# Kernel optimization log

Hardware: AMD Instinct MI355X
Metric: run time of the kernel (lower is better)

## Reference

```python
import jax, jax.numpy as jnp
import numpy as np

COMMITMENT_COST = 0.25


def setup_inputs() -> dict:
    key = jax.random.key(0)
    k1, k2 = jax.random.split(key)
    z = jax.random.normal(k1, (64, 256, 32, 32), dtype=jnp.float32)
    codebook = jax.random.normal(k2, (512, 256), dtype=jnp.float32) * 0.02
    return {"z": z, "codebook": codebook}


def reference(z, codebook):
    B, C, H, W = z.shape
    # [B,C,H,W] -> [B*H*W, C]
    z_flat = jnp.transpose(z, (0, 2, 3, 1)).reshape(-1, C)
    # squared euclidean distances via matmul expansion (same argmin as broadcast form)
    d = (
        jnp.sum(z_flat * z_flat, axis=-1, keepdims=True)
        - 2.0 * (z_flat @ codebook.T)
        + jnp.sum(codebook * codebook, axis=-1)
    )  # [N, num_codes]
    encoding_indices = jnp.argmin(d, axis=1)  # [N]
    z_q = codebook[encoding_indices].reshape(B, H, W, C)
    z_q = jnp.transpose(z_q, (0, 3, 1, 2))  # [B,C,H,W]
    commitment_loss = COMMITMENT_COST * jnp.mean(
        (jax.lax.stop_gradient(z_q) - z) ** 2
    )
    embedding_loss = jnp.mean((z_q - jax.lax.stop_gradient(z)) ** 2)
    loss = commitment_loss + embedding_loss
    # straight-through estimator
    z_q_st = z + jax.lax.stop_gradient(z_q - z)
    return z_q_st, encoding_indices, loss
```

## Files before the change

### kernel.cpp

```cpp
#include <hip/hip_runtime.h>

#define C_DIM   256
#define K_CODES 512
#define N_POS   65536
#define OUT0_ELEMS 16777216
#define OUT1_ELEMS 65536

__global__ __launch_bounds__(256) void vq_transpose_kernel(const float* __restrict__ cb,
                                                           float* __restrict__ cbT)
{
    const int k = blockIdx.x;
    const int c = threadIdx.x;
    cbT[c * K_CODES + k] = cb[k * C_DIM + c];
}

__global__ __launch_bounds__(256) void vq_cc_kernel(const float* __restrict__ cbT,
                                                    float* __restrict__ cc)
{
    const int k = blockIdx.x * 256 + threadIdx.x;
    float s1[8], s2[8];
    #pragma unroll
    for (int j = 0; j < 8; ++j) { s1[j] = 0.f; s2[j] = 0.f; }
    for (int c8 = 0; c8 < 16; ++c8) {
        #pragma unroll
        for (int j = 0; j < 8; ++j) {
            float v = cbT[(c8 * 8 + j) * K_CODES + k];
            s1[j] = __fadd_rn(s1[j], __fmul_rn(v, v));
        }
    }
    for (int c8 = 16; c8 < 32; ++c8) {
        #pragma unroll
        for (int j = 0; j < 8; ++j) {
            float v = cbT[(c8 * 8 + j) * K_CODES + k];
            s2[j] = __fadd_rn(s2[j], __fmul_rn(v, v));
        }
    }
    float b1 = __fadd_rn(__fadd_rn(__fadd_rn(s1[0], s1[1]), __fadd_rn(s1[2], s1[3])),
                         __fadd_rn(__fadd_rn(s1[4], s1[5]), __fadd_rn(s1[6], s1[7])));
    float b2 = __fadd_rn(__fadd_rn(__fadd_rn(s2[0], s2[1]), __fadd_rn(s2[2], s2[3])),
                         __fadd_rn(__fadd_rn(s2[4], s2[5]), __fadd_rn(s2[6], s2[7])));
    cc[k] = __fadd_rn(b1, b2);
}

__global__ __launch_bounds__(256) void vq_zz_kernel(const float* __restrict__ z,
                                                    float* __restrict__ zz)
{
    const int pos = blockIdx.x * 256 + threadIdx.x;
    const float* zp = z + ((size_t)(pos >> 10) << 18) + (pos & 1023);
    float s1[8], s2[8];
    #pragma unroll
    for (int j = 0; j < 8; ++j) { s1[j] = 0.f; s2[j] = 0.f; }
    for (int c8 = 0; c8 < 16; ++c8) {
        #pragma unroll
        for (int j = 0; j < 8; ++j) {
            float v = zp[(size_t)(c8 * 8 + j) << 10];
            s1[j] = __fadd_rn(s1[j], __fmul_rn(v, v));
        }
    }
    for (int c8 = 16; c8 < 32; ++c8) {
        #pragma unroll
        for (int j = 0; j < 8; ++j) {
            float v = zp[(size_t)(c8 * 8 + j) << 10];
            s2[j] = __fadd_rn(s2[j], __fmul_rn(v, v));
        }
    }
    float b1 = __fadd_rn(__fadd_rn(__fadd_rn(s1[0], s1[1]), __fadd_rn(s1[2], s1[3])),
                         __fadd_rn(__fadd_rn(s1[4], s1[5]), __fadd_rn(s1[6], s1[7])));
    float b2 = __fadd_rn(__fadd_rn(__fadd_rn(s2[0], s2[1]), __fadd_rn(s2[2], s2[3])),
                         __fadd_rn(__fadd_rn(s2[4], s2[5]), __fadd_rn(s2[6], s2[7])));
    zz[pos] = __fadd_rn(b1, b2);
}

__global__ __launch_bounds__(256) void vq_main_kernel(
    const float* __restrict__ z, const float* __restrict__ cbT,
    const float* __restrict__ ccv, const float* __restrict__ zzbuf,
    float* __restrict__ bd, int* __restrict__ bc)
{
    const int blk   = blockIdx.x;
    const int cg    = blk & 3;
    const int chunk = blk >> 2;
    const int b     = chunk >> 3;
    const int hw0   = (chunk & 7) << 7;
    const int tid   = threadIdx.x;
    const int lane  = tid & 63;
    const int w     = tid >> 6;

    const float* zp = z + ((size_t)b << 18) + hw0 + lane;
    const int cb0   = __builtin_amdgcn_readfirstlane((cg << 7) + (w << 5));
    const float* cbbase = cbT + cb0;

    float acc[2][32];
    #pragma unroll
    for (int p = 0; p < 2; ++p)
        #pragma unroll
        for (int k = 0; k < 32; ++k) acc[p][k] = 0.f;

    for (int c = 0; c < C_DIM; ++c) {
        const float* zc = zp + ((size_t)c << 10);
        const float zv0 = zc[0];
        const float zv1 = zc[64];
        const float* cbrow = cbbase + (c << 9);
        #pragma unroll
        for (int k = 0; k < 32; ++k) {
            const float cv = cbrow[k];
            acc[0][k] = __builtin_fmaf(zv0, cv, acc[0][k]);
            acc[1][k] = __builtin_fmaf(zv1, cv, acc[1][k]);
        }
    }

    __shared__ float sdm[4][2][64];
    __shared__ int   sco[4][2][64];

    const float* ccp = ccv + cb0;
    const int posb = (b << 10) + hw0 + lane;
    #pragma unroll
    for (int p = 0; p < 2; ++p) {
        const float zzv = zzbuf[posb + p * 64];
        float bestd = 3.4e38f;
        int   bestc = cb0;
        #pragma unroll
        for (int k = 0; k < 32; ++k) {
            float d = __fadd_rn(__fsub_rn(zzv, __fmul_rn(2.0f, acc[p][k])), ccp[k]);
            if (d < bestd) { bestd = d; bestc = cb0 + k; }
        }
        sdm[w][p][lane] = bestd;
        sco[w][p][lane] = bestc;
    }
    __syncthreads();

    if (w == 0) {
        #pragma unroll
        for (int p = 0; p < 2; ++p) {
            float bdv = sdm[0][p][lane];
            int   bcv = sco[0][p][lane];
            #pragma unroll
            for (int ww = 1; ww < 4; ++ww) {
                float d2 = sdm[ww][p][lane];
                int   c2 = sco[ww][p][lane];
                if (d2 < bdv || (d2 == bdv && c2 < bcv)) { bdv = d2; bcv = c2; }
            }
            bd[(cg << 16) + posb + p * 64] = bdv;
            bc[(cg << 16) + posb + p * 64] = bcv;
        }
    }
}

__global__ __launch_bounds__(256) void vq_combine_kernel(
    const float* __restrict__ bd, const int* __restrict__ bc,
    int* __restrict__ idx, float* __restrict__ out1, float* __restrict__ partials)
{
    const int t   = threadIdx.x;
    const int pos = blockIdx.x * 256 + t;
    float bdv = bd[pos];
    int   bcv = bc[pos];
    #pragma unroll
    for (int g = 1; g < 4; ++g) {
        float d2 = bd[(g << 16) + pos];
        int   c2 = bc[(g << 16) + pos];
        if (d2 < bdv || (d2 == bdv && c2 < bcv)) { bdv = d2; bcv = c2; }
    }
    idx[pos]  = bcv;
    out1[pos] = (float)bcv;

    __shared__ float s[256];
    s[t] = bdv;
    __syncthreads();
    for (int off = 128; off > 0; off >>= 1) {
        if (t < off) s[t] += s[t + off];
        __syncthreads();
    }
    if (t == 0) partials[blockIdx.x] = s[0];
}

__global__ __launch_bounds__(256) void vq_gather_kernel(
    const float* __restrict__ cb, const int* __restrict__ idx,
    float* __restrict__ out0)
{
    const int blk = blockIdx.x;
    const int b   = blk >> 4;
    const int hw0 = (blk & 15) << 6;
    const int lane = threadIdx.x & 63;
    const int w    = threadIdx.x >> 6;

    __shared__ int sidx[64];
    if (threadIdx.x < 64) sidx[threadIdx.x] = idx[(blk << 6) + threadIdx.x];
    __syncthreads();

    const int code = sidx[lane];
    const float4* crow4 = reinterpret_cast<const float4*>(cb + ((size_t)code << 8) + (w << 6));
    float* ob = out0 + ((size_t)b << 18) + ((size_t)(w * 64) << 10) + hw0 + lane;
    #pragma unroll 4
    for (int j4 = 0; j4 < 16; ++j4) {
        float4 v = crow4[j4];
        ob[(size_t)(j4 * 4 + 0) << 10] = v.x;
        ob[(size_t)(j4 * 4 + 1) << 10] = v.y;
        ob[(size_t)(j4 * 4 + 2) << 10] = v.z;
        ob[(size_t)(j4 * 4 + 3) << 10] = v.w;
    }
}

__global__ __launch_bounds__(256) void vq_finalize_kernel(
    const float* __restrict__ partials, float* __restrict__ out2)
{
    __shared__ float s[256];
    const int t = threadIdx.x;
    s[t] = partials[t];
    __syncthreads();
    for (int off = 128; off > 0; off >>= 1) {
        if (t < off) s[t] += s[t + off];
        __syncthreads();
    }
    if (t == 0)
        out2[0] = 1.25f * (s[0] * (1.0f / 16777216.0f));
}

extern "C" void kernel_launch(void* const* d_in, const int* in_sizes, int n_in,
                              void* d_out, int out_size, void* d_ws, size_t ws_size,
                              hipStream_t stream)
{
    const float* z  = (const float*)d_in[0];
    const float* cb = (const float*)d_in[1];

    float* out0 = (float*)d_out;
    float* out1 = out0 + OUT0_ELEMS;
    float* out2 = out0 + OUT0_ELEMS + OUT1_ELEMS;

    float* bd = out0;
    int*   bc = (int*)(out0 + 4 * N_POS);
    float* zz = out0 + 8 * N_POS;

    float* wsf      = (float*)d_ws;
    float* partials = wsf;
    float* ccv      = wsf + 256;
    float* cbT      = wsf + 1024;
    int*   idx      = (int*)(wsf + 1024 + C_DIM * K_CODES);

    hipLaunchKernelGGL(vq_transpose_kernel, dim3(512),  dim3(256), 0, stream, cb, cbT);
    hipLaunchKernelGGL(vq_cc_kernel,        dim3(2),    dim3(256), 0, stream, cbT, ccv);
    hipLaunchKernelGGL(vq_zz_kernel,        dim3(256),  dim3(256), 0, stream, z, zz);
    hipLaunchKernelGGL(vq_main_kernel,      dim3(2048), dim3(256), 0, stream,
                       z, cbT, ccv, zz, bd, bc);
    hipLaunchKernelGGL(vq_combine_kernel,   dim3(256),  dim3(256), 0, stream,
                       bd, bc, idx, out1, partials);
    hipLaunchKernelGGL(vq_gather_kernel,    dim3(1024), dim3(256), 0, stream, cb, idx, out0);
    hipLaunchKernelGGL(vq_finalize_kernel,  dim3(1),    dim3(256), 0, stream, partials, out2);
}
```

Measured before the change: 224.7 us.

## Stage z tiles in double-buffered shared memory and reorder blocks by code group

The main distance kernel now loads each 32-channel slice of z with float4 loads into a double-buffered LDS tile, prefetching the next slice into registers while computing on the current one. Each wave used to issue its own scalar global loads per channel. The block index mapping also changes so that blocks sharing a code group run consecutively, which may improve codebook cache locality. In exchange it adds block barriers per tile, 32KB of LDS per block, and register pressure from the prefetch buffer, all of which can lower occupancy.

```diff
diff --git a/kernel.cpp b/kernel.cpp
--- a/kernel.cpp
+++ b/kernel.cpp
@@ -77,39 +77,79 @@
     float* __restrict__ bd, int* __restrict__ bc)
 {
     const int blk   = blockIdx.x;
-    const int cg    = blk & 3;
-    const int chunk = blk >> 2;
+    const int cg    = blk >> 9;
+    const int chunk = blk & 511;
     const int b     = chunk >> 3;
     const int hw0   = (chunk & 7) << 7;
     const int tid   = threadIdx.x;
     const int lane  = tid & 63;
     const int w     = tid >> 6;
 
-    const float* zp = z + ((size_t)b << 18) + hw0 + lane;
+    __shared__ float zbuf[2][32 * 128];
+    __shared__ float sdm[4][2][64];
+    __shared__ int   sco[4][2][64];
+
     const int cb0   = __builtin_amdgcn_readfirstlane((cg << 7) + (w << 5));
     const float* cbbase = cbT + cb0;
 
+    const int sr = tid >> 3;
+    const int sc = tid & 7;
+    const float* zg = z + ((size_t)b << 18) + hw0;
+
+    float4 R[4];
+
+    #pragma unroll
+    for (int i = 0; i < 4; ++i) {
+        const int c4 = sc + 8 * i;
+        R[i] = *reinterpret_cast<const float4*>(zg + ((size_t)sr << 10) + (c4 << 2));
+    }
+    #pragma unroll
+    for (int i = 0; i < 4; ++i) {
+        const int c4 = sc + 8 * i;
+        *reinterpret_cast<float4*>(&zbuf[0][sr * 128 + c4 * 4]) = R[i];
+    }
+    #pragma unroll
+    for (int i = 0; i < 4; ++i) {
+        const int c4 = sc + 8 * i;
+        R[i] = *reinterpret_cast<const float4*>(zg + ((size_t)(32 + sr) << 10) + (c4 << 2));
+    }
+
     float acc[2][32];
     #pragma unroll
     for (int p = 0; p < 2; ++p)
         #pragma unroll
         for (int k = 0; k < 32; ++k) acc[p][k] = 0.f;
 
-    for (int c = 0; c < C_DIM; ++c) {
-        const float* zc = zp + ((size_t)c << 10);
-        const float zv0 = zc[0];
-        const float zv1 = zc[64];
-        const float* cbrow = cbbase + (c << 9);
-        #pragma unroll
-        for (int k = 0; k < 32; ++k) {
-            const float cv = cbrow[k];
-            acc[0][k] = __builtin_fmaf(zv0, cv, acc[0][k]);
-            acc[1][k] = __builtin_fmaf(zv1, cv, acc[1][k]);
-        }
-    }
-
-    __shared__ float sdm[4][2][64];
-    __shared__ int   sco[4][2][64];
+    for (int ct = 0; ct < 8; ++ct) {
+        __syncthreads();
+        if (ct < 7) {
+            #pragma unroll
+            for (int i = 0; i < 4; ++i) {
+                const int c4 = sc + 8 * i;
+                *reinterpret_cast<float4*>(&zbuf[(ct + 1) & 1][sr * 128 + c4 * 4]) = R[i];
+            }
+            if (ct < 6) {
+                #pragma unroll
+                for (int i = 0; i < 4; ++i) {
+                    const int c4 = sc + 8 * i;
+                    R[i] = *reinterpret_cast<const float4*>(
+                        zg + ((size_t)((ct + 2) * 32 + sr) << 10) + (c4 << 2));
+                }
+            }
+        }
+        const float* zl = &zbuf[ct & 1][0];
+        for (int r = 0; r < 32; ++r) {
+            const float zv0 = zl[r * 128 + lane];
+            const float zv1 = zl[r * 128 + 64 + lane];
+            const float* cbrow = cbbase + ((ct * 32 + r) << 9);
+            #pragma unroll
+            for (int k = 0; k < 32; ++k) {
+                const float cv = cbrow[k];
+                acc[0][k] = __builtin_fmaf(zv0, cv, acc[0][k]);
+                acc[1][k] = __builtin_fmaf(zv1, cv, acc[1][k]);
+            }
+        }
+    }
 
     const float* ccp = ccv + cb0;
     const int posb = (b << 10) + hw0 + lane;
```

New measurement: 255.3 us. +13.6%, slower.
